# Kernel tuning notes

Hardware: AMD Instinct MI355X
Metric: run time of the kernel (lower is better)

## Reference

```python
import jax, jax.numpy as jnp
import numpy as np

N, D, H, HD, R, K, TM = 32768, 128, 2, 64, 2, 32, 2
E_EDGES, M_MOTIFS, NG = 262144, 131072, 32
EPS = 1e-5
BETA_MAX = 5.0
GRAD_CLIP = 1.0
STATE_CLIP = 10.0
DAMPING = 1.0

def _isp(x):
    # inverse softplus of init values (params stored pre-softplus)
    return float(np.log(np.expm1(x)))

LAM2_RAW, LAM3_RAW, LAMM_RAW = _isp(1.0), _isp(0.5), _isp(1.0)
B2_RAW, B3_RAW, BM_RAW = _isp(1.0), _isp(1.0), _isp(1.0)


def layernorm(x, g, b):
    mu = x.mean(-1, keepdims=True)
    v = ((x - mu) ** 2).mean(-1, keepdims=True)
    return g * (x - mu) * jax.lax.rsqrt(v + EPS) + b


def seg_lse(s, seg, n, beta):
    # tempered logsumexp over segments: (1/beta) log sum_j exp(beta*s_j); s:[items,H] -> [n,H]
    sb = beta * s
    m = jax.ops.segment_max(sb, seg, num_segments=n)
    m = jnp.where(jnp.isfinite(m), m, 0.0)
    z = jax.ops.segment_sum(jnp.exp(sb - m[seg]), seg, num_segments=n)
    return jnp.where(z > 0, (m + jnp.log(jnp.maximum(z, 1e-30))) / beta, 0.0)


def energy(X, a_2, ln_gamma, ln_beta, W_Q2, W_K2, W_Q3, W_K3, T_tau, W_Qm, W_Km, B_mem,
           c_2, u_2, c_3, u_3, v_3, t_tau, batch):
    sp = jax.nn.softplus
    lam2, lam3, lamm = sp(LAM2_RAW), sp(LAM3_RAW), sp(LAMM_RAW)
    b2 = jnp.minimum(sp(B2_RAW), BETA_MAX)
    b3 = jnp.minimum(sp(B3_RAW), BETA_MAX)
    bm = jnp.minimum(sp(BM_RAW), BETA_MAX)
    G = layernorm(X, ln_gamma, ln_beta)
    # pairwise Q2/K2 term over edges (c_2 <- u_2) with learned per-edge bias a_2
    Q2 = jnp.einsum('nd,hzd->nhz', G, W_Q2)  # [N,H,HD]
    K2 = jnp.einsum('nd,hzd->nhz', G, W_K2)
    s2 = jnp.einsum('ehz,ehz->eh', Q2[c_2], K2[u_2]) / np.sqrt(HD) + a_2  # [E,H]
    e_pair = -lam2 * seg_lse(s2, c_2, N, b2).sum(-1)  # [N]
    # rank-R bilinear motif term over (c_3,u_3,v_3) with type embedding T_tau
    Q3 = jnp.einsum('nd,hzd->nhz', G, W_Q3).reshape(N, H, R, HD)
    K3 = jnp.einsum('nd,hzd->nhz', G, W_K3).reshape(N, H, R, HD)
    qk = jnp.einsum('mhrz,mhrz->mhr', Q3[c_3], K3[u_3])
    tv = jnp.einsum('mhrz,mhrz->mhr', T_tau[t_tau], K3[v_3])
    s3 = (qk * tv).sum(-1) / HD  # [M,H]
    e_motif = -lam3 * seg_lse(s3, c_3, N, b3).sum(-1)
    # K-slot memory term
    Qm = jnp.einsum('nd,hzd->nhz', G, W_Qm)
    Km = jnp.einsum('kd,hzd->hkz', B_mem, W_Km)
    sm = jnp.einsum('nhz,hkz->nhk', Qm, Km) / np.sqrt(HD)
    e_mem = -(lamm / bm) * jax.nn.logsumexp(bm * sm, axis=-1).sum(-1)
    e_node = 0.5 * (X * X).sum(-1) + e_pair + e_motif + e_mem
    return jax.ops.segment_sum(e_node, batch, num_segments=NG)  # per-graph energy [NG]


def setup_inputs() -> dict:
    key = jax.random.key(0)
    ks = jax.random.split(key, 16)
    inp = {}
    inp['X'] = jax.random.normal(ks[0], (N, D), jnp.float32)
    inp['c_2'] = jax.random.randint(ks[1], (E_EDGES,), 0, N)
    inp['u_2'] = jax.random.randint(ks[2], (E_EDGES,), 0, N)
    inp['c_3'] = jax.random.randint(ks[3], (M_MOTIFS,), 0, N)
    inp['u_3'] = jax.random.randint(ks[4], (M_MOTIFS,), 0, N)
    inp['v_3'] = jax.random.randint(ks[5], (M_MOTIFS,), 0, N)
    inp['t_tau'] = jax.random.randint(ks[6], (M_MOTIFS,), 0, TM)
    inp['batch'] = jnp.sort(jax.random.randint(ks[7], (N,), 0, NG))
    inp['a_2'] = 0.1 * jax.random.normal(ks[8], (E_EDGES, H), jnp.float32)
    inp['step_size'] = jnp.full((1,), 0.1, jnp.float32)
    inp['ln_gamma'] = jnp.ones((D,), jnp.float32)
    inp['ln_beta'] = jnp.zeros((D,), jnp.float32)
    s = 1.0 / np.sqrt(D)
    inp['W_Q2'] = s * jax.random.normal(ks[9], (H, HD, D), jnp.float32)
    inp['W_K2'] = s * jax.random.normal(ks[10], (H, HD, D), jnp.float32)
    inp['W_Q3'] = 0.5 * s * jax.random.normal(ks[11], (H, R * HD, D), jnp.float32)
    inp['W_K3'] = 0.5 * s * jax.random.normal(ks[12], (H, R * HD, D), jnp.float32)
    inp['T_tau'] = 0.02 * jax.random.normal(ks[13], (TM, H, R, HD), jnp.float32)
    inp['W_Qm'] = 0.5 * s * jax.random.normal(ks[14], (H, HD, D), jnp.float32)
    inp['W_Km'] = 0.5 * s * jax.random.normal(ks[15], (H, HD, D), jnp.float32)
    inp['B_mem'] = s * jax.random.normal(jax.random.fold_in(key, 99), (K, D), jnp.float32)
    return inp


def reference(X, c_2, u_2, c_3, u_3, v_3, t_tau, batch, a_2, step_size,
              ln_gamma, ln_beta, W_Q2, W_K2, W_Q3, W_K3, T_tau, W_Qm, W_Km, B_mem):
    Eg, vjp = jax.vjp(
        lambda Xv: energy(Xv, a_2, ln_gamma, ln_beta, W_Q2, W_K2, W_Q3, W_K3, T_tau,
                          W_Qm, W_Km, B_mem, c_2, u_2, c_3, u_3, v_3, t_tau, batch), X)
    gX, = vjp(jnp.ones_like(Eg))
    gnorm = jnp.linalg.norm(gX, axis=-1, keepdims=True)
    gX = gX * (GRAD_CLIP / jnp.maximum(gnorm, GRAD_CLIP))
    X_next = X - step_size[0] * DAMPING * gX
    snorm = jnp.linalg.norm(X_next, axis=-1, keepdims=True)
    X_next = X_next * (STATE_CLIP / jnp.maximum(snorm, STATE_CLIP))
    return X_next, Eg
```

## Files before the change

### kernel.cpp

```cpp
#include <hip/hip_runtime.h>
#include <hip/hip_bf16.h>
#include <math.h>

typedef __hip_bfloat16 bf16;
typedef short bf16x8 __attribute__((ext_vector_type(8)));
typedef float f32x4 __attribute__((ext_vector_type(4)));

#define N_NODES 32768
#define D_DIM 128
#define E_EDG 262144
#define M_MOT 131072
#define NG_G 32
#define F_TOT 832

__device__ __forceinline__ int pidx(int n){ return ((n & 7) << 12) | (n >> 3); }

__device__ __forceinline__ float wsum64(float v){
#pragma unroll
  for (int o = 32; o > 0; o >>= 1) v += __shfl_xor(v, o, 64);
  return v;
}
__device__ __forceinline__ float hsum32(float v){
#pragma unroll
  for (int o = 16; o > 0; o >>= 1) v += __shfl_xor(v, o, 64);
  return v;
}
__device__ __forceinline__ float hmax32(float v){
#pragma unroll
  for (int o = 16; o > 0; o >>= 1) v = fmaxf(v, __shfl_xor(v, o, 64));
  return v;
}
__device__ __forceinline__ float hsum8(float v){
#pragma unroll
  for (int o = 4; o > 0; o >>= 1) v += __shfl_xor(v, o, 64);
  return v;
}
__device__ __forceinline__ float bflo(unsigned u){ return __uint_as_float(u << 16); }
__device__ __forceinline__ float bfhi(unsigned u){ return __uint_as_float(u & 0xffff0000u); }
__device__ __forceinline__ unsigned packbf(float x, float y){
  bf16 a = __float2bfloat16(x), b = __float2bfloat16(y);
  unsigned short ua = *(unsigned short*)&a, ub = *(unsigned short*)&b;
  return (unsigned)ua | ((unsigned)ub << 16);
}
__device__ __forceinline__ void unpk8(uint4 p, float* f){
  f[0] = bflo(p.x); f[1] = bfhi(p.x); f[2] = bflo(p.y); f[3] = bfhi(p.y);
  f[4] = bflo(p.z); f[5] = bfhi(p.z); f[6] = bflo(p.w); f[7] = bfhi(p.w);
}

__global__ __launch_bounds__(256) void k_phaseA(
    const int* c2, const int* u2, const int* c3, const int* u3, const int* v3,
    const float* wq2, const float* wk2, const float* wq3, const float* wk3,
    const float* wqm, const float* wkm, const float* bmem, const float* Ttau,
    int* cnt, float* Wcat, bf16* Ttb, float* Mprod){
  __shared__ float KmL[64];
  int b = blockIdx.x, t = threadIdx.x;
  if (b < 1024){
    int* base = cnt + (size_t)(b & 7) * 5 * N_NODES;
    int i = b * 256 + t;
    atomicAdd(&base[pidx(c2[i])], 1);
    atomicAdd(&base[N_NODES + pidx(u2[i])], 1);
    if (i < M_MOT){
      atomicAdd(&base[2 * N_NODES + pidx(c3[i])], 1);
      atomicAdd(&base[3 * N_NODES + pidx(u3[i])], 1);
      atomicAdd(&base[4 * N_NODES + pidx(v3[i])], 1);
    }
  } else if (b < 1440){
    int idx = (b - 1024) * 256 + t;
    if (idx < 768 * D_DIM){
      int f = idx / D_DIM, d = idx - f * D_DIM;
      const float* src; int fr;
      if      (f < 128){ src = wq2; fr = f; }
      else if (f < 256){ src = wk2; fr = f - 128; }
      else if (f < 512){ src = wq3; fr = f - 256; }
      else             { src = wk3; fr = f - 512; }
      Wcat[f * D_DIM + d] = src[fr * D_DIM + d];
    } else {
      int j = idx - 768 * D_DIM;
      Ttb[j] = __float2bfloat16(Ttau[j]);
    }
  } else {
    int hk = b - 1440;
    int h = hk >> 5, k = hk & 31;
    if (t < 64){
      const float* wrow = wkm + (size_t)(h * 64 + t) * D_DIM;
      const float* brow = bmem + k * D_DIM;
      float acc = 0.f;
      for (int d = 0; d < D_DIM; d++) acc += wrow[d] * brow[d];
      KmL[t] = acc;
    }
    __syncthreads();
    if (t < 128){
      const float* w = wqm + (size_t)(h * 64) * 128 + t;
      float acc = 0.f;
      for (int z = 0; z < 64; z++) acc += w[z * 128] * KmL[z];
      Mprod[t * 64 + hk] = acc;
    }
  }
}

__global__ __launch_bounds__(256) void k_reduce8(int* cnt){
  int idx = blockIdx.x * 256 + threadIdx.x;
  int4* base = (int4*)cnt;
  int4 s = base[idx];
#pragma unroll
  for (int rr = 1; rr < 8; rr++){
    int4 v = *(const int4*)(cnt + (size_t)rr * 5 * N_NODES + 4 * (size_t)idx);
    s.x += v.x; s.y += v.y; s.z += v.z; s.w += v.w;
  }
  base[idx] = s;
}

__global__ __launch_bounds__(1024) void k_phaseB(
    int* cntcur, int* off,
    const float* X, const float* gamma, const float* beta,
    bf16* Gb, float* mu, float* rstd, float* e_node,
    const float* Wcat, const float* Mprod, bf16* wfF, bf16* wfB){
  __shared__ int sd[1024];
  int b = blockIdx.x, t = threadIdx.x;
  if (b < 5){
    int* c = cntcur + b * N_NODES;
    int* o = off + b * (N_NODES + 1);
    int4 lv[8];
    const int4* c4 = (const int4*)c;
#pragma unroll
    for (int j4 = 0; j4 < 8; j4++) lv[j4] = c4[t * 8 + j4];
    int* lvp = (int*)lv;
    int loc[32];
    int sum = 0;
#pragma unroll
    for (int j = 0; j < 32; j++){ loc[j] = sum; sum += lvp[j]; }
    sd[t] = sum;
    __syncthreads();
    for (int s = 1; s < 1024; s <<= 1){
      int v = (t >= s) ? sd[t - s] : 0;
      __syncthreads();
      sd[t] += v;
      __syncthreads();
    }
    int excl = sd[t] - sum;
#pragma unroll
    for (int j = 0; j < 32; j++){
      int val = excl + loc[j];
      o[t * 32 + j] = val;
      c[t * 32 + j] = val;
    }
    if (t == 1023) o[N_NODES] = sd[1023];
  } else if (b < 2053){
    int wv = t >> 6, l = t & 63;
    int n = (b - 5) * 16 + wv;
    float2 x2 = ((const float2*)(X + (size_t)n * 128))[l];
    float sumx = wsum64(x2.x + x2.y);
    float sumxx = wsum64(x2.x * x2.x + x2.y * x2.y);
    float m = sumx * (1.0f / 128.0f);
    float var = sumxx * (1.0f / 128.0f) - m * m;
    float rs = rsqrtf(var + 1e-5f);
    float2 gg = ((const float2*)gamma)[l];
    float2 bb = ((const float2*)beta)[l];
    ((unsigned*)(Gb + (size_t)n * 128))[l] =
        packbf(gg.x * (x2.x - m) * rs + bb.x, gg.y * (x2.y - m) * rs + bb.y);
    if (l == 0){ mu[n] = m; rstd[n] = rs; e_node[n] = 0.5f * sumxx; }
  } else {
    int idx = (b - 2053) * 1024 + t;
    int j = idx & 7, lane = (idx >> 3) & 63, tt = idx >> 9;
    {
      int tn = tt >> 2, kt = tt & 3;
      int f = tn * 16 + (lane & 15), d = kt * 32 + (lane >> 4) * 8 + j;
      float v = (f < 768) ? Wcat[f * 128 + d] : 0.125f * Mprod[d * 64 + (f - 768)];
      wfF[idx] = __float2bfloat16(v);
    }
    {
      int td = tt / 26, tf = tt - td * 26;
      int f = tf * 32 + (lane >> 4) * 8 + j, d = td * 16 + (lane & 15);
      float v = (f < 768) ? Wcat[f * 128 + d] : -0.125f * Mprod[d * 64 + (f - 768)];
      wfB[idx] = __float2bfloat16(v);
    }
  }
}

__global__ __launch_bounds__(256) void k_phaseC(
    const bf16* Gb, const bf16* wfF, bf16* P,
    const int* c2, const int* u2, const int* c3, const int* u3, const int* v3,
    const int* t3, int* cur,
    uint2* lec, uint2* leu, uint2* lmc, uint2* lmu, uint2* lmv){
  int b = blockIdx.x;
  int g = b / 29, r = b - g * 29;
  if (r < 13){
    __shared__ unsigned shP[64 * 36];
    int f = g * 13 + r;
    int bx = f & 511, by = f >> 9;
    int wave = threadIdx.x >> 6, lane = threadIdx.x & 63;
    int m0 = bx * 64 + wave * 16;
    int tn0 = by * 4;
    int rw = lane & 15, quad = lane >> 4;
    const bf16* aptr = Gb + (size_t)(m0 + rw) * 128 + quad * 8;
    bf16x8 a[4];
#pragma unroll
    for (int kt = 0; kt < 4; kt++) a[kt] = *(const bf16x8*)(aptr + kt * 32);
    f32x4 acc[4];
#pragma unroll
    for (int i = 0; i < 4; i++) acc[i] = (f32x4){0.f, 0.f, 0.f, 0.f};
#pragma unroll
    for (int nf = 0; nf < 4; nf++){
      int tn = tn0 + nf;
#pragma unroll
      for (int kt = 0; kt < 4; kt++){
        bf16x8 bb = *(const bf16x8*)(wfF + (((size_t)tn * 4 + kt) * 64 + lane) * 8);
        acc[nf] = __builtin_amdgcn_mfma_f32_16x16x32_bf16(bb, a[kt], acc[nf], 0, 0, 0);
      }
    }
    int lrow = wave * 16 + rw;
#pragma unroll
    for (int nf = 0; nf < 4; nf++){
      unsigned lo = packbf(acc[nf][0], acc[nf][1]);
      unsigned hi = packbf(acc[nf][2], acc[nf][3]);
      *(uint2*)&shP[lrow * 36 + nf * 8 + quad * 2] = make_uint2(lo, hi);
    }
    __syncthreads();
    int t = threadIdx.x;
    int orow = t >> 2, s = t & 3;
    uint4 v0 = *(const uint4*)&shP[orow * 36 + s * 4];
    uint4 v1 = *(const uint4*)&shP[orow * 36 + 16 + s * 4];
    uint4* prow = (uint4*)(P + (size_t)(bx * 64 + orow) * F_TOT) + tn0 * 2 + s;
    prow[0] = v0;
    prow[4] = v1;
  } else {
    int j = g * 16 + (r - 13);
    int range = j >> 3;
    int res = b & 7;
    int i = range * 256 + threadIdx.x;
    {
      int c = c2[i], u = u2[i];
      if ((c & 7) == res){
        int pos = atomicAdd(&cur[pidx(c)], 1);
        lec[pos] = make_uint2((unsigned)u, (unsigned)i);
      }
      if ((u & 7) == res){
        int pos = atomicAdd(&cur[N_NODES + pidx(u)], 1);
        leu[pos] = make_uint2((unsigned)c, (unsigned)i);
      }
    }
    if (i < M_MOT){
      int c = c3[i], u = u3[i], v = v3[i], mt = t3[i];
      if ((c & 7) == res){
        int pos = atomicAdd(&cur[2 * N_NODES + pidx(c)], 1);
        lmc[pos] = make_uint2((unsigned)(u | (v << 16)), (unsigned)(mt | (i << 5)));
      }
      if ((u & 7) == res){
        int pos = atomicAdd(&cur[3 * N_NODES + pidx(u)], 1);
        lmu[pos] = make_uint2((unsigned)c, (unsigned)i);
      }
      if ((v & 7) == res){
        int pos = atomicAdd(&cur[4 * N_NODES + pidx(v)], 1);
        lmv[pos] = make_uint2((unsigned)(c | (mt << 16)), (unsigned)i);
      }
    }
  }
}

__global__ __launch_bounds__(256) void k_fused_c(const bf16* P, const uint2* lec, const uint2* lmc,
                   const bf16* Ttb, const float* a2, const int* off_ec, const int* off_mc,
                   float* s2, float* rz2, float* s3, float* qkb, float* tvb, float* rz3,
                   bf16* dP, float* e_pair, float* e_mot, float* e_mem){
  int b = blockIdx.x;
  int type = b % 3, grp = b / 3;
  int wave = threadIdx.x >> 6, z = threadIdx.x & 63;
  int n = grp * 4 + wave;
  int l = z & 31, lh = z >> 5;
  int pn = pidx(n);

  if (type == 0){
    int q = z >> 4, l16 = z & 15, hg = l16 >> 3;
    int beg = off_ec[pn], end = off_ec[pn + 1];
    uint4 qp = ((const uint4*)(P + (size_t)n * F_TOT))[l16];
    float qv[8]; unpk8(qp, qv);
    float acc[8] = {0,0,0,0,0,0,0,0};
    float zz = 0.f;
    int iters = (end - beg + 3) >> 2;
    for (int it = 0; it < iters; it++){
      int idx = beg + 4 * it + q;
      bool valid = idx < end;
      int idc = valid ? idx : end - 1;
      uint2 pl = lec[idc];
      float2 av = *(const float2*)(a2 + (size_t)pl.y * 2);
      uint4 kp = ((const uint4*)(P + (size_t)pl.x * F_TOT + 128))[l16];
      float kv[8]; unpk8(kp, kv);
      float d = 0.f;
#pragma unroll
      for (int j = 0; j < 8; j++) d += qv[j] * kv[j];
      float s = hsum8(d) * 0.125f + (hg ? av.y : av.x);
      if (valid && (l16 & 7) == 0) s2[2 * pl.y + hg] = s;
      float ex = valid ? __expf(s) : 0.f;
#pragma unroll
      for (int j = 0; j < 8; j++) acc[j] += ex * kv[j];
      zz += ex;
    }
#pragma unroll
    for (int j = 0; j < 8; j++){
      acc[j] += __shfl_xor(acc[j], 16, 64);
      acc[j] += __shfl_xor(acc[j], 32, 64);
    }
    zz += __shfl_xor(zz, 16, 64);
    zz += __shfl_xor(zz, 32, 64);
    float rz = (zz > 0.f) ? 1.0f / zz : 0.f;
    float coef = -0.125f * rz;
    if (z < 16){
      uint4 o;
      o.x = packbf(coef * acc[0], coef * acc[1]);
      o.y = packbf(coef * acc[2], coef * acc[3]);
      o.z = packbf(coef * acc[4], coef * acc[5]);
      o.w = packbf(coef * acc[6], coef * acc[7]);
      ((uint4*)(dP + (size_t)n * F_TOT))[l16] = o;
      if ((l16 & 7) == 0) rz2[n * 2 + hg] = rz;
    }
    float eterm = (zz > 0.f) ? -__logf(zz) : 0.f;
    float eo = __shfl(eterm, 8, 64);
    if (z == 0) e_pair[n] = eterm + eo;
  } else if (type == 1){
    int g = l >> 3, hg = g >> 1;
    int beg = off_mc[pn], end = off_mc[pn + 1];
    uint4 qp = ((const uint4*)(P + (size_t)n * F_TOT + 256))[l];
    float qv[8]; unpk8(qp, qv);
    float acc[8] = {0,0,0,0,0,0,0,0};
    float zz = 0.f;
    int iters = (end - beg + 1) >> 1;
    for (int it = 0; it < iters; it++){
      int idx = beg + 2 * it + lh;
      bool valid = idx < end;
      int idc = valid ? idx : end - 1;
      uint2 pl = lmc[idc];
      int u = pl.x & 0xffff, v = pl.x >> 16;
      int tix = pl.y & 31; unsigned m = pl.y >> 5;
      uint4 kup = ((const uint4*)(P + (size_t)u * F_TOT + 512))[l];
      uint4 kvp = ((const uint4*)(P + (size_t)v * F_TOT + 512))[l];
      uint4 tp  = ((const uint4*)(Ttb + (size_t)tix * 256))[l];
      float k[8], vv[8], pt[8];
      unpk8(kup, k); unpk8(kvp, vv); unpk8(tp, pt);
      float dq = 0.f, dt = 0.f;
#pragma unroll
      for (int j = 0; j < 8; j++){ dq += qv[j] * k[j]; dt += pt[j] * vv[j]; }
      float qk = hsum8(dq);
      float tv = hsum8(dt);
      if (valid && (l & 7) == 0){ qkb[(size_t)4 * m + g] = qk; tvb[(size_t)4 * m + g] = tv; }
      float w = qk * tv;
      float s = (w + __shfl_xor(w, 8, 64)) * (1.0f / 64.0f);
      if (valid && (l & 15) == 0) s3[2 * m + hg] = s;
      float ex = valid ? __expf(s) : 0.f;
      float et = ex * tv;
#pragma unroll
      for (int j = 0; j < 8; j++) acc[j] += et * k[j];
      zz += ex;
    }
#pragma unroll
    for (int j = 0; j < 8; j++) acc[j] += __shfl_xor(acc[j], 32, 64);
    zz += __shfl_xor(zz, 32, 64);
    float rz = (zz > 0.f) ? 1.0f / zz : 0.f;
    float coef = (-0.5f / 64.0f) * rz;
    if (z < 32){
      uint4 o;
      o.x = packbf(coef * acc[0], coef * acc[1]);
      o.y = packbf(coef * acc[2], coef * acc[3]);
      o.z = packbf(coef * acc[4], coef * acc[5]);
      o.w = packbf(coef * acc[6], coef * acc[7]);
      ((uint4*)(dP + (size_t)n * F_TOT + 256))[l] = o;
      if ((l & 15) == 0) rz3[n * 2 + hg] = rz;
    }
    float eterm = (zz > 0.f) ? -0.5f * __logf(zz) : 0.f;
    float eo = __shfl(eterm, 16, 64);
    if (z == 0) e_mot[n] = eterm + eo;
  } else {
    unsigned short us = ((const unsigned short*)(P + (size_t)n * F_TOT + 768))[z];
    float s = __uint_as_float((unsigned)us << 16);
    float mx = hmax32(s);
    float ex = __expf(s - mx);
    float se = hsum32(ex);
    float p = ex / se;
    bf16 pb = __float2bfloat16(p);
    ((unsigned short*)(dP + (size_t)n * F_TOT + 768))[z] = *(unsigned short*)&pb;
    float eterm = -(mx + __logf(se));
    float eo = __shfl(eterm, z ^ 32, 64);
    if (z == 0) e_mem[n] = eterm + eo;
  }
}

__global__ __launch_bounds__(256) void k_phaseE(const bf16* P, const uint2* leu,
                    const uint2* lmu, const uint2* lmv, const bf16* Ttb,
                    const float* s2, const float* rz2, const float* s3, const float* rz3,
                    const float* qkb, const float* tvb,
                    const int* off_eu, const int* off_mu, const int* off_mv, bf16* dP,
                    const float* e_node, const float* e_pair, const float* e_mot,
                    const float* e_mem, const int* batch, float* Eg){
  __shared__ float eg[NG_G];
  int b = blockIdx.x;
  if (b < 128){
    int t = threadIdx.x;
    if (t < NG_G) eg[t] = 0.f;
    __syncthreads();
    int n = b * 256 + t;
    float e = e_node[n] + e_pair[n] + e_mot[n] + e_mem[n];
    atomicAdd(&eg[batch[n]], e);
    __syncthreads();
    if (t < NG_G) atomicAdd(&Eg[t], eg[t]);
    return;
  }
  int b2 = b - 128;
  int type = b2 & 1, grp = b2 >> 1;
  int wave = threadIdx.x >> 6, z = threadIdx.x & 63;
  int n = grp * 4 + wave;
  int pn = pidx(n);

  if (type == 0){
    int e8 = z >> 3, l8 = z & 7;
    int beg = off_eu[pn], end = off_eu[pn + 1];
    float acc[16];
#pragma unroll
    for (int j = 0; j < 16; j++) acc[j] = 0.f;
    int iters = (end - beg + 7) >> 3;
    for (int it = 0; it < iters; it++){
      int idx = beg + 8 * it + e8;
      bool valid = idx < end;
      int idc = valid ? idx : end - 1;
      uint2 pl = leu[idc];
      const uint4* qrow = (const uint4*)(P + (size_t)pl.x * F_TOT);
      uint4 qp0 = qrow[l8];
      uint4 qp1 = qrow[l8 + 8];
      float2 sv = *(const float2*)(s2 + 2 * (size_t)pl.y);
      float2 rv = *(const float2*)(rz2 + 2 * (size_t)pl.x);
      float qv0[8], qv1[8];
      unpk8(qp0, qv0); unpk8(qp1, qv1);
      float p0 = valid ? __expf(sv.x) * rv.x : 0.f;
      float p1 = valid ? __expf(sv.y) * rv.y : 0.f;
#pragma unroll
      for (int j = 0; j < 8; j++){
        acc[j]     += p0 * qv0[j];
        acc[8 + j] += p1 * qv1[j];
      }
    }
#pragma unroll
    for (int j = 0; j < 16; j++){
      acc[j] += __shfl_xor(acc[j], 8, 64);
      acc[j] += __shfl_xor(acc[j], 16, 64);
      acc[j] += __shfl_xor(acc[j], 32, 64);
    }
    if (z < 8){
      uint4 o0, o1;
      o0.x = packbf(-0.125f * acc[0], -0.125f * acc[1]);
      o0.y = packbf(-0.125f * acc[2], -0.125f * acc[3]);
      o0.z = packbf(-0.125f * acc[4], -0.125f * acc[5]);
      o0.w = packbf(-0.125f * acc[6], -0.125f * acc[7]);
      o1.x = packbf(-0.125f * acc[8], -0.125f * acc[9]);
      o1.y = packbf(-0.125f * acc[10], -0.125f * acc[11]);
      o1.z = packbf(-0.125f * acc[12], -0.125f * acc[13]);
      o1.w = packbf(-0.125f * acc[14], -0.125f * acc[15]);
      uint4* dst = (uint4*)(dP + (size_t)n * F_TOT + 128);
      dst[z] = o0;
      dst[z + 8] = o1;
    }
  } else {
    int m4 = z >> 4, l16 = z & 15;
    int g0 = l16 >> 3;
    float acc[16];
#pragma unroll
    for (int j = 0; j < 16; j++) acc[j] = 0.f;
    {
      int beg = off_mu[pn], end = off_mu[pn + 1];
      int iters = (end - beg + 3) >> 2;
      for (int it = 0; it < iters; it++){
        int idx = beg + 4 * it + m4;
        bool valid = idx < end;
        int idc = valid ? idx : end - 1;
        uint2 pl = lmu[idc];
        const uint4* qrow = (const uint4*)(P + (size_t)pl.x * F_TOT + 256);
        uint4 qp0 = qrow[l16];
        uint4 qp1 = qrow[l16 + 16];
        float2 sv = *(const float2*)(s3 + 2 * (size_t)pl.y);
        float2 rv = *(const float2*)(rz3 + 2 * (size_t)pl.x);
        float4 tq = *(const float4*)(tvb + 4 * (size_t)pl.y);
        float t0 = g0 ? tq.y : tq.x;
        float t1 = g0 ? tq.w : tq.z;
        float qv0[8], qv1[8];
        unpk8(qp0, qv0); unpk8(qp1, qv1);
        float w0 = valid ? __expf(sv.x) * rv.x * t0 : 0.f;
        float w1 = valid ? __expf(sv.y) * rv.y * t1 : 0.f;
#pragma unroll
        for (int j = 0; j < 8; j++){
          acc[j]     += w0 * qv0[j];
          acc[8 + j] += w1 * qv1[j];
        }
      }
    }
    {
      int beg = off_mv[pn], end = off_mv[pn + 1];
      int iters = (end - beg + 3) >> 2;
      for (int it = 0; it < iters; it++){
        int idx = beg + 4 * it + m4;
        bool valid = idx < end;
        int idc = valid ? idx : end - 1;
        uint2 pl = lmv[idc];
        unsigned c = pl.x & 0xffff, tix = pl.x >> 16;
        const uint4* trow = (const uint4*)(Ttb + (size_t)tix * 256);
        uint4 tp0 = trow[l16];
        uint4 tp1 = trow[l16 + 16];
        float2 sv = *(const float2*)(s3 + 2 * (size_t)pl.y);
        float2 rv = *(const float2*)(rz3 + 2 * (size_t)c);
        float4 qq = *(const float4*)(qkb + 4 * (size_t)pl.y);
        float q0 = g0 ? qq.y : qq.x;
        float q1 = g0 ? qq.w : qq.z;
        float pt0[8], pt1[8];
        unpk8(tp0, pt0); unpk8(tp1, pt1);
        float w0 = valid ? __expf(sv.x) * rv.x * q0 : 0.f;
        float w1 = valid ? __expf(sv.y) * rv.y * q1 : 0.f;
#pragma unroll
        for (int j = 0; j < 8; j++){
          acc[j]     += w0 * pt0[j];
          acc[8 + j] += w1 * pt1[j];
        }
      }
    }
#pragma unroll
    for (int j = 0; j < 16; j++){
      acc[j] += __shfl_xor(acc[j], 16, 64);
      acc[j] += __shfl_xor(acc[j], 32, 64);
    }
    const float cst = -0.5f / 64.0f;
    if (z < 16){
      uint4 o0, o1;
      o0.x = packbf(cst * acc[0], cst * acc[1]);
      o0.y = packbf(cst * acc[2], cst * acc[3]);
      o0.z = packbf(cst * acc[4], cst * acc[5]);
      o0.w = packbf(cst * acc[6], cst * acc[7]);
      o1.x = packbf(cst * acc[8], cst * acc[9]);
      o1.y = packbf(cst * acc[10], cst * acc[11]);
      o1.z = packbf(cst * acc[12], cst * acc[13]);
      o1.w = packbf(cst * acc[14], cst * acc[15]);
      uint4* dst = (uint4*)(dP + (size_t)n * F_TOT + 512);
      dst[l16] = o0;
      dst[l16 + 16] = o1;
    }
  }
}

__global__ __launch_bounds__(256) void k_bwd_mfma(const bf16* dP, const bf16* wfB, float* dG){
  int wave = threadIdx.x >> 6, lane = threadIdx.x & 63;
  int m0 = blockIdx.x * 64 + wave * 16;
  int rw = lane & 15, quad = lane >> 4;
  const bf16* aptr = dP + (size_t)(m0 + rw) * F_TOT + quad * 8;
  f32x4 acc[8];
#pragma unroll
  for (int i = 0; i < 8; i++) acc[i] = (f32x4){0.f, 0.f, 0.f, 0.f};
  for (int kt = 0; kt < 26; kt++){
    bf16x8 a = *(const bf16x8*)(aptr + kt * 32);
#pragma unroll
    for (int td = 0; td < 8; td++){
      bf16x8 b = *(const bf16x8*)(wfB + (((size_t)td * 26 + kt) * 64 + lane) * 8);
      acc[td] = __builtin_amdgcn_mfma_f32_16x16x32_bf16(a, b, acc[td], 0, 0, 0);
    }
  }
#pragma unroll
  for (int td = 0; td < 8; td++){
    int col = td * 16 + rw;
#pragma unroll
    for (int r = 0; r < 4; r++){
      int row = m0 + quad * 4 + r;
      dG[(size_t)row * 128 + col] = acc[td][r];
    }
  }
}

__global__ __launch_bounds__(256) void k_finalize(const float* X, const float* dG, const float* gamma,
                    const float* mu, const float* rstd, const float* step_p,
                    const float* Eg, float* out){
  int wave = threadIdx.x >> 6, l = threadIdx.x & 63;
  int n = blockIdx.x * 4 + wave;
  float2 x2 = ((const float2*)(X + (size_t)n * 128))[l];
  float2 dg2 = ((const float2*)(dG + (size_t)n * 128))[l];
  float2 gg = ((const float2*)gamma)[l];
  float rs = rstd[n], m = mu[n];
  float xh0 = (x2.x - m) * rs, xh1 = (x2.y - m) * rs;
  float dxh0 = dg2.x * gg.x, dxh1 = dg2.y * gg.y;
  float s1 = wsum64(dxh0 + dxh1);
  float s2v = wsum64(dxh0 * xh0 + dxh1 * xh1);
  float g0 = x2.x + rs * (dxh0 - s1 * (1.0f / 128) - xh0 * (s2v * (1.0f / 128)));
  float g1 = x2.y + rs * (dxh1 - s1 * (1.0f / 128) - xh1 * (s2v * (1.0f / 128)));
  float gn = sqrtf(wsum64(g0 * g0 + g1 * g1));
  float gc = 1.0f / fmaxf(gn, 1.0f);
  g0 *= gc; g1 *= gc;
  float step = step_p[0];
  float xn0 = x2.x - step * g0, xn1 = x2.y - step * g1;
  float sn = sqrtf(wsum64(xn0 * xn0 + xn1 * xn1));
  float sc = 10.0f / fmaxf(sn, 10.0f);
  ((float2*)(out + (size_t)n * 128))[l] = make_float2(xn0 * sc, xn1 * sc);
  if (blockIdx.x == 0 && threadIdx.x < NG_G)
    out[(size_t)N_NODES * 128 + threadIdx.x] = Eg[threadIdx.x];
}

extern "C" void kernel_launch(void* const* d_in, const int* in_sizes, int n_in,
                              void* d_out, int out_size, void* d_ws, size_t ws_size,
                              hipStream_t stream) {
  const float* X     = (const float*)d_in[0];
  const int*  c_2    = (const int*) d_in[1];
  const int*  u_2    = (const int*) d_in[2];
  const int*  c_3    = (const int*) d_in[3];
  const int*  u_3    = (const int*) d_in[4];
  const int*  v_3    = (const int*) d_in[5];
  const int*  t_tau  = (const int*) d_in[6];
  const int*  batch  = (const int*) d_in[7];
  const float* a_2   = (const float*)d_in[8];
  const float* step_s= (const float*)d_in[9];
  const float* ln_g  = (const float*)d_in[10];
  const float* ln_b  = (const float*)d_in[11];
  const float* W_Q2  = (const float*)d_in[12];
  const float* W_K2  = (const float*)d_in[13];
  const float* W_Q3  = (const float*)d_in[14];
  const float* W_K3  = (const float*)d_in[15];
  const float* T_tau = (const float*)d_in[16];
  const float* W_Qm  = (const float*)d_in[17];
  const float* W_Km  = (const float*)d_in[18];
  const float* B_mem = (const float*)d_in[19];
  float* out = (float*)d_out;

  char* wb = (char*)d_ws;
  float* Wcat   = (float*)wb; wb += 768 * D_DIM * 4;
  float* Mprod  = (float*)wb; wb += 8192 * 4;
  float* mu     = (float*)wb; wb += N_NODES * 4;
  float* rstd   = (float*)wb; wb += N_NODES * 4;
  float* s2     = (float*)wb; wb += (size_t)E_EDG * 2 * 4;
  float* rz2    = (float*)wb; wb += N_NODES * 2 * 4;
  float* s3     = (float*)wb; wb += (size_t)M_MOT * 2 * 4;
  float* qkb    = (float*)wb; wb += (size_t)M_MOT * 4 * 4;
  float* tvb    = (float*)wb; wb += (size_t)M_MOT * 4 * 4;
  float* rz3    = (float*)wb; wb += N_NODES * 2 * 4;
  float* e_node = (float*)wb; wb += N_NODES * 4;
  float* e_pair = (float*)wb; wb += N_NODES * 4;
  float* e_mot  = (float*)wb; wb += N_NODES * 4;
  float* e_mem  = (float*)wb; wb += N_NODES * 4;
  float* Eg     = (float*)wb; wb += NG_G * 4;
  float* dG     = (float*)wb; wb += (size_t)N_NODES * D_DIM * 4;
  bf16* Gb      = (bf16*)wb;  wb += (size_t)N_NODES * D_DIM * 2;
  bf16* P       = (bf16*)wb;  wb += (size_t)N_NODES * F_TOT * 2;
  bf16* dP      = (bf16*)wb;  wb += (size_t)N_NODES * F_TOT * 2;
  bf16* wfF     = (bf16*)wb;  wb += 106496 * 2;
  bf16* wfB     = (bf16*)wb;  wb += 106496 * 2;
  bf16* Ttb     = (bf16*)wb;  wb += 8192 * 2;
  int* cntcur   = (int*)wb;   wb += 8 * 5 * N_NODES * 4;
  int* off      = (int*)wb;   wb += 5 * (N_NODES + 1) * 4;
  wb = (char*)(((size_t)wb + 15) & ~(size_t)15);
  uint2* lec    = (uint2*)wb; wb += (size_t)E_EDG * 8;
  uint2* leu    = (uint2*)wb; wb += (size_t)E_EDG * 8;
  uint2* lmc    = (uint2*)wb; wb += (size_t)M_MOT * 8;
  uint2* lmu    = (uint2*)wb; wb += (size_t)M_MOT * 8;
  uint2* lmv    = (uint2*)wb; wb += (size_t)M_MOT * 8;

  const int* off_ec = off;
  const int* off_eu = off + (N_NODES + 1);
  const int* off_mc = off + 2 * (N_NODES + 1);
  const int* off_mu = off + 3 * (N_NODES + 1);
  const int* off_mv = off + 4 * (N_NODES + 1);

  hipMemsetAsync(cntcur, 0, (size_t)8 * 5 * N_NODES * sizeof(int), stream);
  hipMemsetAsync(Eg, 0, NG_G * sizeof(float), stream);
  hipLaunchKernelGGL(k_phaseA, dim3(1504), dim3(256), 0, stream,
                     c_2, u_2, c_3, u_3, v_3, W_Q2, W_K2, W_Q3, W_K3,
                     W_Qm, W_Km, B_mem, T_tau, cntcur, Wcat, Ttb, Mprod);
  hipLaunchKernelGGL(k_reduce8, dim3(160), dim3(256), 0, stream, cntcur);
  hipLaunchKernelGGL(k_phaseB, dim3(2157), dim3(1024), 0, stream,
                     cntcur, off, X, ln_g, ln_b, Gb, mu, rstd, e_node,
                     Wcat, Mprod, wfF, wfB);
  hipLaunchKernelGGL(k_phaseC, dim3(512 * 29), dim3(256), 0, stream,
                     Gb, wfF, P, c_2, u_2, c_3, u_3, v_3, t_tau, cntcur,
                     lec, leu, lmc, lmu, lmv);
  hipLaunchKernelGGL(k_fused_c, dim3(3 * (N_NODES / 4)), dim3(256), 0, stream,
                     P, lec, lmc, Ttb, a_2, off_ec, off_mc,
                     s2, rz2, s3, qkb, tvb, rz3, dP, e_pair, e_mot, e_mem);
  hipLaunchKernelGGL(k_phaseE, dim3(128 + 2 * (N_NODES / 4)), dim3(256), 0, stream,
                     P, leu, lmu, lmv, Ttb, s2, rz2, s3, rz3, qkb, tvb,
                     off_eu, off_mu, off_mv, dP,
                     e_node, e_pair, e_mot, e_mem, batch, Eg);
  hipLaunchKernelGGL(k_bwd_mfma, dim3(N_NODES / 64), dim3(256), 0, stream, dP, wfB, dG);
  hipLaunchKernelGGL(k_finalize, dim3(N_NODES / 4), dim3(256), 0, stream,
                     X, dG, ln_g, mu, rstd, step_s, Eg, out);
}
```

Baseline: 370.0 us.

## Precompute per-node type-embedding dot products with MFMA for motif tv term

Adds a kernel that, for every node and every type-slot entry (32 rows of Ttb, apparently TM×H×R padded), computes the dot product of T_tau with the node's K3 slice using bf16 MFMA, and stores the results in a dense TV4 table. The motif loop in the fused kernel then reads one float4 from TV4 instead of gathering the 64-wide K3 row of v and the T row and reducing them. This trades a per-motif gather and reduction for a per-node dense precompute plus an extra 16 MB buffer written and read back. It also adds one more launch.

```diff
diff --git a/kernel.cpp b/kernel.cpp
--- a/kernel.cpp
+++ b/kernel.cpp
@@ -257,8 +257,54 @@
   }
 }
 
+__global__ __launch_bounds__(256) void k_tv(const bf16* P, const bf16* Ttb, float* TV4){
+  __shared__ float sh[64 * 132];
+  int blk = blockIdx.x;
+  int wave = threadIdx.x >> 6, lane = threadIdx.x & 63;
+  int rw = lane & 15, quad = lane >> 4;
+  int m0 = blk * 64 + wave * 16;
+  const bf16* kbase = P + (size_t)(m0 + rw) * F_TOT + 512 + quad * 8;
+#pragma unroll
+  for (int hr = 0; hr < 4; hr++){
+    bf16x8 a0 = *(const bf16x8*)(kbase + hr * 64);
+    bf16x8 a1 = *(const bf16x8*)(kbase + hr * 64 + 32);
+    f32x4 acc0 = (f32x4){0.f,0.f,0.f,0.f};
+    f32x4 acc1 = (f32x4){0.f,0.f,0.f,0.f};
+    {
+      const bf16* tb = Ttb + (size_t)rw * 256 + hr * 64 + quad * 8;
+      bf16x8 t0 = *(const bf16x8*)(tb);
+      bf16x8 t1 = *(const bf16x8*)(tb + 32);
+      acc0 = __builtin_amdgcn_mfma_f32_16x16x32_bf16(t0, a0, acc0, 0, 0, 0);
+      acc0 = __builtin_amdgcn_mfma_f32_16x16x32_bf16(t1, a1, acc0, 0, 0, 0);
+    }
+    {
+      const bf16* tb = Ttb + (size_t)(16 + rw) * 256 + hr * 64 + quad * 8;
+      bf16x8 t0 = *(const bf16x8*)(tb);
+      bf16x8 t1 = *(const bf16x8*)(tb + 32);
+      acc1 = __builtin_amdgcn_mfma_f32_16x16x32_bf16(t0, a0, acc1, 0, 0, 0);
+      acc1 = __builtin_amdgcn_mfma_f32_16x16x32_bf16(t1, a1, acc1, 0, 0, 0);
+    }
+    int lrow = wave * 16 + rw;
+#pragma unroll
+    for (int r_ = 0; r_ < 4; r_++){
+      sh[lrow * 132 + (quad * 4 + r_) * 4 + hr] = acc0[r_];
+      sh[lrow * 132 + (16 + quad * 4 + r_) * 4 + hr] = acc1[r_];
+    }
+  }
+  __syncthreads();
+  int t = threadIdx.x;
+#pragma unroll
+  for (int it = 0; it < 8; it++){
+    int idx4 = it * 256 + t;
+    int node = idx4 >> 5, toff = (idx4 & 31) * 4;
+    float4 v = *(const float4*)&sh[node * 132 + toff];
+    ((float4*)TV4)[(size_t)blk * 2048 + idx4] = v;
+  }
+}
+
 __global__ __launch_bounds__(256) void k_fused_c(const bf16* P, const uint2* lec, const uint2* lmc,
-                   const bf16* Ttb, const float* a2, const int* off_ec, const int* off_mc,
+                   const bf16* Ttb, const float* TV4, const float* a2,
+                   const int* off_ec, const int* off_mc,
                    float* s2, float* rz2, float* s3, float* qkb, float* tvb, float* rz3,
                    bf16* dP, float* e_pair, float* e_mot, float* e_mem){
   int b = blockIdx.x;
@@ -331,15 +377,14 @@
       int u = pl.x & 0xffff, v = pl.x >> 16;
       int tix = pl.y & 31; unsigned m = pl.y >> 5;
       uint4 kup = ((const uint4*)(P + (size_t)u * F_TOT + 512))[l];
-      uint4 kvp = ((const uint4*)(P + (size_t)v * F_TOT + 512))[l];
-      uint4 tp  = ((const uint4*)(Ttb + (size_t)tix * 256))[l];
-      float k[8], vv[8], pt[8];
-      unpk8(kup, k); unpk8(kvp, vv); unpk8(tp, pt);
-      float dq = 0.f, dt = 0.f;
-#pragma unroll
-      for (int j = 0; j < 8; j++){ dq += qv[j] * k[j]; dt += pt[j] * vv[j]; }
+      float4 tvv = ((const float4*)TV4)[(size_t)v * 32 + tix];
+      float tv = (g & 2) ? ((g & 1) ? tvv.w : tvv.z) : ((g & 1) ? tvv.y : tvv.x);
+      float k[8];
+      unpk8(kup, k);
+      float dq = 0.f;
+#pragma unroll
+      for (int j = 0; j < 8; j++) dq += qv[j] * k[j];
       float qk = hsum8(dq);
-      float tv = hsum8(dt);
       if (valid && (l & 7) == 0){ qkb[(size_t)4 * m + g] = qk; tvb[(size_t)4 * m + g] = tv; }
       float w = qk * tv;
       float s = (w + __shfl_xor(w, 8, 64)) * (1.0f / 64.0f);
@@ -635,6 +680,7 @@
   float* e_mem  = (float*)wb; wb += N_NODES * 4;
   float* Eg     = (float*)wb; wb += NG_G * 4;
   float* dG     = (float*)wb; wb += (size_t)N_NODES * D_DIM * 4;
+  float* TV4    = (float*)wb; wb += (size_t)N_NODES * 32 * 4 * 4;
   bf16* Gb      = (bf16*)wb;  wb += (size_t)N_NODES * D_DIM * 2;
   bf16* P       = (bf16*)wb;  wb += (size_t)N_NODES * F_TOT * 2;
   bf16* dP      = (bf16*)wb;  wb += (size_t)N_NODES * F_TOT * 2;
@@ -668,8 +714,9 @@
   hipLaunchKernelGGL(k_phaseC, dim3(512 * 29), dim3(256), 0, stream,
                      Gb, wfF, P, c_2, u_2, c_3, u_3, v_3, t_tau, cntcur,
                      lec, leu, lmc, lmu, lmv);
+  hipLaunchKernelGGL(k_tv, dim3(512), dim3(256), 0, stream, P, Ttb, TV4);
   hipLaunchKernelGGL(k_fused_c, dim3(3 * (N_NODES / 4)), dim3(256), 0, stream,
-                     P, lec, lmc, Ttb, a_2, off_ec, off_mc,
+                     P, lec, lmc, Ttb, TV4, a_2, off_ec, off_mc,
                      s2, rz2, s3, qkb, tvb, rz3, dP, e_pair, e_mot, e_mem);
   hipLaunchKernelGGL(k_phaseE, dim3(128 + 2 * (N_NODES / 4)), dim3(256), 0, stream,
                      P, leu, lmu, lmv, Ttb, s2, rz2, s3, rz3, qkb, tvb,
```

Measured after the change: 374.8 us. No clear change (+1.3%).
